# Kernel tuning notes

Measured on AMD Instinct MI355X. Metric: run time of the kernel, lower is better.

## Reference

```python
import jax, jax.numpy as jnp
import numpy as np

B, H, D = 2048, 50, 400          # batch, history_length, news/category embed dim
S, C = 285, 18                   # num_subcategories, num_categories
NC = 50                          # num_clicks_embed_dim (= history_length table size)
FILL = 1e-30                     # masked_fill value used by the original module


def setup_inputs() -> dict:
    key = jax.random.key(0)
    ks = jax.random.split(key, 9)
    vectors = jax.random.normal(ks[0], (B, H, D), dtype=jnp.float32)
    subcategory = jax.random.randint(ks[1], (B, H), 0, S, dtype=jnp.int32)
    category = jax.random.randint(ks[2], (B, H), 0, C, dtype=jnp.int32)
    subcat_embed = jax.random.normal(ks[3], (S, D), dtype=jnp.float32) * 0.02
    cat_embed = jax.random.normal(ks[4], (C, D), dtype=jnp.float32) * 0.02
    clicks_embed = jax.random.normal(ks[5], (H, NC), dtype=jnp.float32) * 0.02
    w_news = jax.random.normal(ks[6], (D,), dtype=jnp.float32) * 0.05
    w_subcat = jax.random.normal(ks[7], (D + NC,), dtype=jnp.float32) * 0.05
    w_cat = jax.random.normal(ks[8], (D + NC,), dtype=jnp.float32) * 0.05
    return {"vectors": vectors, "subcategory": subcategory, "category": category,
            "subcat_embed": subcat_embed, "cat_embed": cat_embed,
            "clicks_embed": clicks_embed, "w_news": w_news,
            "w_subcat": w_subcat, "w_cat": w_cat}


def reference(vectors, subcategory, category, subcat_embed, cat_embed,
              clicks_embed, w_news, w_subcat, w_cat):
    sub_mask = jax.nn.one_hot(subcategory, S, dtype=vectors.dtype)   # [B,H,S]
    cat_mask = jax.nn.one_hot(category, C, dtype=vectors.dtype)      # [B,H,C]
    sub_to_cat = jnp.einsum('bhs,bhc->bsc', sub_mask, cat_mask)      # [B,S,C]

    # --- news -> subcategory attention pooling ---
    news_scores = jnp.einsum('bhd,d->bh', vectors, w_news)           # [B,H]
    scores = jnp.where(sub_mask > 0, news_scores[:, :, None], FILL)  # [B,H,S]
    news_w = jax.nn.softmax(scores, axis=1)
    sub_news_repr = jnp.einsum('bhs,bhd->bsd', news_w, vectors)      # [B,S,D]
    sub_repr = sub_news_repr + subcat_embed[None]                    # [B,S,D]

    sub_clicks = sub_mask.sum(axis=1)                                # [B,S] float counts
    sub_weights = sub_clicks / sub_clicks.sum(axis=1, keepdims=True)
    sub_clicks_emb = clicks_embed[sub_clicks.astype(jnp.int32)]      # [B,S,NC]

    # --- subcategory -> category attention pooling ---
    sc_scores = jnp.einsum('bsk,k->bs',
                           jnp.concatenate([sub_repr, sub_clicks_emb], axis=2),
                           w_subcat)                                 # [B,S]
    scores2 = jnp.where(sub_to_cat > 0, sc_scores[:, :, None], FILL) # [B,S,C]
    sub_w = jax.nn.softmax(scores2, axis=1)
    cat_sub_repr = jnp.einsum('bsc,bsd->bcd', sub_w, sub_repr)       # [B,C,D]
    cat_repr = cat_sub_repr + cat_embed[None]                        # [B,C,D]

    cat_clicks = cat_mask.sum(axis=1)                                # [B,C]
    cat_weights = cat_clicks / cat_clicks.sum(axis=1, keepdims=True)
    cat_clicks_emb = clicks_embed[cat_clicks.astype(jnp.int32)]      # [B,C,NC]

    # --- category -> user attention pooling (unmasked) ---
    c_scores = jnp.einsum('bck,k->bc',
                          jnp.concatenate([cat_repr, cat_clicks_emb], axis=2),
                          w_cat)                                     # [B,C]
    cat_w = jax.nn.softmax(c_scores, axis=1)
    user_repr = jnp.einsum('bc,bcd->bd', cat_w, cat_repr)            # [B,D]

    return (sub_repr, sub_weights, cat_repr, cat_weights, user_repr)
```

## Files before the change

### kernel.cpp

```cpp
#include <hip/hip_runtime.h>

#define BB 2048
#define HH 50
#define DD 400
#define D4 100
#define SS 285
#define CC 18
#define NCC 50
#define FILLV 1e-30f

static constexpr int BLOCK = 256;
static constexpr int TOT4 = SS * D4;

static constexpr size_t OFF1 = (size_t)BB * SS * DD;
static constexpr size_t OFF2 = OFF1 + (size_t)BB * SS;
static constexpr size_t OFF3 = OFF2 + (size_t)BB * CC * DD;
static constexpr size_t OFF4 = OFF3 + (size_t)BB * CC;

#define WS_ETOT 0
#define WS_SCE  400
#define WS_SEW  688
#define WS_CEDS 976
#define WS_CEDC 1026
#define WS_CEW  1076

typedef float f4 __attribute__((ext_vector_type(4)));

__global__ void hierec_pre(const float* __restrict__ subcat_embed,
                           const float* __restrict__ cat_embed,
                           const float* __restrict__ clicks_embed,
                           const float* __restrict__ w_subcat,
                           const float* __restrict__ w_cat,
                           float* __restrict__ ws)
{
    const int tid  = threadIdx.x;
    const int lane = tid & 63;
    const int wave = tid >> 6;
    const int wpb  = blockDim.x >> 6;
    const int gw   = blockIdx.x * wpb + wave;
    const int nw   = gridDim.x * wpb;

    for (int s = gw; s < SS; s += nw) {
        float p1 = 0.f, p2 = 0.f;
        for (int d = lane; d < DD; d += 64) {
            float v = subcat_embed[s * DD + d];
            p1 += v * w_subcat[d];
            p2 += v * w_cat[d];
        }
        for (int off = 32; off; off >>= 1) {
            p1 += __shfl_down(p1, off);
            p2 += __shfl_down(p2, off);
        }
        if (lane == 0) { ws[WS_SCE + s] = p1; ws[WS_SEW + s] = p2; }
    }
    if (blockIdx.x == 0) {
        for (int d = tid; d < DD; d += blockDim.x) {
            float a = 0.f;
            for (int s = 0; s < SS; ++s) a += subcat_embed[s * DD + d];
            ws[WS_ETOT + d] = a;
        }
    }
    if (blockIdx.x == 1) {
        for (int k = wave; k < HH; k += wpb) {
            float p1 = 0.f, p2 = 0.f;
            if (lane < NCC) {
                float v = clicks_embed[k * NCC + lane];
                p1 = v * w_subcat[DD + lane];
                p2 = v * w_cat[DD + lane];
            }
            for (int off = 32; off; off >>= 1) {
                p1 += __shfl_down(p1, off);
                p2 += __shfl_down(p2, off);
            }
            if (lane == 0) { ws[WS_CEDS + k] = p1; ws[WS_CEDC + k] = p2; }
        }
    }
    if (blockIdx.x == 2) {
        for (int c = wave; c < CC; c += wpb) {
            float p = 0.f;
            for (int d = lane; d < DD; d += 64) p += cat_embed[c * DD + d] * w_cat[d];
            for (int off = 32; off; off >>= 1) p += __shfl_down(p, off);
            if (lane == 0) ws[WS_CEW + c] = p;
        }
    }
}

__global__ __launch_bounds__(BLOCK, 8) void hierec_main(
    const float* __restrict__ vectors,
    const int*   __restrict__ subcategory,
    const int*   __restrict__ category,
    const float* __restrict__ subcat_embed,
    const float* __restrict__ cat_embed,
    const float* __restrict__ w_news,
    const float* __restrict__ w_subcat,
    const float* __restrict__ w_cat,
    const float* __restrict__ pre,
    float* __restrict__ out)
{
    const int b    = blockIdx.x;
    const int tid  = threadIdx.x;
    const int lane = tid & 63;
    const int wave = tid >> 6;

    __shared__ f4     vt4L[D4];
    __shared__ f4     et4L[D4];
    __shared__ float  coefS[SS];
    __shared__ unsigned long long maskS[SS];
    __shared__ int    cntS[SS];
    __shared__ float  ns1L[HH], ns2L[HH], ns3L[HH];
    __shared__ float  uzL[HH], wNL[HH], scL[HH];
    __shared__ unsigned long long maskL[HH];
    __shared__ int    hsL[HH], hcL[HH], repL[HH], prepL[HH];
    __shared__ float  GmL[CC][HH];
    __shared__ float  mcL[CC], ucL[CC], rZcL[CC], AL[CC], csL[CC], catwL[CC];
    __shared__ int    cntcL[CC];
    __shared__ int    prepCL[HH], prepSL[HH], prepJL[HH];
    __shared__ float  prepGL[HH], uPL[HH], uGL[HH];
    __shared__ int    npL;
    __shared__ float  PvL, vtwL, etwL, uAL, uEL;

    const float* vb  = vectors + (size_t)b * HH * DD;
    const f4*    vb4 = (const f4*)vb;
    const f4*    se4 = (const f4*)subcat_embed;
    const f4*    ce4 = (const f4*)cat_embed;

    if (tid < HH) {
        hsL[tid] = subcategory[b * HH + tid];
        hcL[tid] = category[b * HH + tid];
    }
    for (int s = tid; s < SS; s += BLOCK) {
        coefS[s] = 1.f / (float)HH;
        maskS[s] = 0ull;
        cntS[s]  = 0;
    }
    __syncthreads();

    for (int h = wave; h < HH; h += 4) {
        float p1 = 0.f, p2 = 0.f, p3 = 0.f;
        for (int d = lane; d < DD; d += 64) {
            float v = vb[h * DD + d];
            p1 += v * w_news[d];
            p2 += v * w_subcat[d];
            p3 += v * w_cat[d];
        }
        for (int off = 32; off; off >>= 1) {
            p1 += __shfl_down(p1, off);
            p2 += __shfl_down(p2, off);
            p3 += __shfl_down(p3, off);
        }
        if (lane == 0) { ns1L[h] = p1; ns2L[h] = p2; ns3L[h] = p3; }
    }
    if (tid < D4) {
        f4 a = {0.f, 0.f, 0.f, 0.f};
        #pragma unroll 5
        for (int h = 0; h < HH; ++h) a += vb4[h * D4 + tid];
        vt4L[tid] = a;
        et4L[tid] = ((const f4*)pre)[tid];
    }
    __syncthreads();

    if (tid < HH) {
        const int h = tid;
        const int s = hsL[h], c = hcL[h];
        unsigned long long mask = 0ull, pmask = 0ull;
        for (int j = 0; j < HH; ++j) {
            bool ms = (hsL[j] == s);
            mask  |= (unsigned long long)(ms ? 1 : 0) << j;
            pmask |= (unsigned long long)((ms && hcL[j] == c) ? 1 : 0) << j;
        }
        int cnt = __popcll(mask);
        bool rep = ((__ffsll((long long)mask) - 1) == h);

        float m = FILLV;
        unsigned long long t = mask;
        while (t) { int j = __ffsll((long long)t) - 1; t &= t - 1; m = fmaxf(m, ns1L[j]); }
        float u = expf(FILLV - m);
        float sumE = 0.f, sum2 = 0.f;
        t = mask;
        while (t) {
            int j = __ffsll((long long)t) - 1; t &= t - 1;
            float e = expf(ns1L[j] - m);
            sumE += e;
            sum2 += (e - u) * ns2L[j];
        }
        float Z = sumE + (float)(HH - cnt) * u;
        float vt2 = 0.f;
        for (int j = 0; j < HH; ++j) vt2 += ns2L[j];
        int ci = cnt < (NCC - 1) ? cnt : (NCC - 1);
        float sc = (sum2 + u * vt2) / Z + pre[WS_SCE + s] + pre[WS_CEDS + ci];

        float e_h = expf(ns1L[h] - m);
        float uz = u / Z;
        wNL[h] = (e_h - u) / Z;
        uzL[h] = uz; maskL[h] = mask; scL[h] = sc;
        repL[h]  = rep ? 1 : 0;
        prepL[h] = ((__ffsll((long long)pmask) - 1) == h) ? 1 : 0;
        if (rep) { coefS[s] = uz; maskS[s] = mask; cntS[s] = cnt; }
    } else if (wave == 1) {
        float p = 0.f;
        const float* et = (const float*)et4L;
        for (int d = lane; d < DD; d += 64) p += et[d] * w_cat[d];
        for (int off = 32; off; off >>= 1) p += __shfl_down(p, off);
        if (lane == 0) etwL = p;
    } else if (wave == 2) {
        float p = (lane < HH) ? ns3L[lane] : 0.f;
        for (int off = 32; off; off >>= 1) p += __shfl_down(p, off);
        if (lane == 0) vtwL = p;
    }
    __syncthreads();

    if (tid < CC) {
        const int c = tid;
        float mc = FILLV; int n = 0, cc2 = 0;
        for (int j = 0; j < HH; ++j) {
            if (hcL[j] == c) ++cc2;
            if (prepL[j] && hcL[j] == c) { ++n; mc = fmaxf(mc, scL[j]); }
        }
        float u = expf(FILLV - mc);
        float sumE = 0.f;
        for (int j = 0; j < HH; ++j)
            if (prepL[j] && hcL[j] == c) sumE += expf(scL[j] - mc);
        float Zc = sumE + (float)(SS - n) * u;
        mcL[c] = mc; ucL[c] = u; rZcL[c] = 1.f / Zc; cntcL[c] = cc2;
        __builtin_nontemporal_store((float)cc2 * (1.f / (float)HH),
                                    &out[OFF3 + (size_t)b * CC + c]);
    }
    if (tid == 64) {
        int nd = 0, np = 0;
        float sumUb = 0.f;
        for (int j = 0; j < HH; ++j) {
            if (repL[j]) { ++nd; sumUb += uzL[j]; }
            if (prepL[j]) { prepCL[np] = hcL[j]; prepSL[np] = hsL[j]; prepJL[np] = j; ++np; }
        }
        npL = np;
        PvL = (float)(SS - nd) * (1.f / (float)HH) + sumUb;
    }
    for (int s = tid; s < SS; s += BLOCK)
        __builtin_nontemporal_store((float)cntS[s] * (1.f / (float)HH),
                                    &out[OFF1 + (size_t)b * SS + s]);
    __syncthreads();

    for (int idx = tid; idx < CC * HH; idx += BLOCK) {
        int c = idx / HH, h = idx - c * HH;
        bool exists = false;
        unsigned long long t = maskL[h];
        while (t) {
            int k = __ffsll((long long)t) - 1; t &= t - 1;
            if (hcL[k] == c) { exists = true; break; }
        }
        float g = exists ? (expf(scL[h] - mcL[c]) - ucL[c]) : 0.f;
        GmL[c][h] = wNL[h] * (ucL[c] + g);
    }
    if (tid < CC) {
        const int c = tid;
        float A = ucL[c] * PvL;
        for (int j = 0; j < HH; ++j)
            if (prepL[j] && hcL[j] == c)
                A += (expf(scL[j] - mcL[c]) - ucL[c]) * uzL[j];
        AL[c] = A;
    }
    __syncthreads();
    if (tid >= 64 && tid < 64 + HH) {
        int jj = tid - 64;
        if (jj < npL) {
            int j = prepJL[jj], c = prepCL[jj];
            prepGL[jj] = expf(scL[j] - mcL[c]) - ucL[c];
        }
    }
    __syncthreads();

    if (tid < CC) {
        const int c = tid;
        float sG = 0.f;
        for (int h = 0; h < HH; ++h) sG += GmL[c][h] * ns3L[h];
        float sP = 0.f;
        const int np = npL;
        for (int jj = 0; jj < np; ++jj)
            if (prepCL[jj] == c) sP += prepGL[jj] * pre[WS_SEW + prepSL[jj]];
        int ci = cntcL[c] < (NCC - 1) ? cntcL[c] : (NCC - 1);
        csL[c] = rZcL[c] * (AL[c] * vtwL + ucL[c] * etwL + sG + sP)
                 + pre[WS_CEW + c] + pre[WS_CEDC + ci];
    }
    __syncthreads();

    if (tid < CC) {
        float m = csL[0];
        for (int j = 1; j < CC; ++j) m = fmaxf(m, csL[j]);
        float Zc = 0.f;
        for (int j = 0; j < CC; ++j) Zc += expf(csL[j] - m);
        catwL[tid] = expf(csL[tid] - m) / Zc;
    }
    __syncthreads();
    if (tid < HH) {
        float g = 0.f;
        for (int c = 0; c < CC; ++c) g += catwL[c] * rZcL[c] * GmL[c][tid];
        uGL[tid] = g;
    }
    if (tid == 64) {
        float uA = 0.f, uE = 0.f;
        for (int c = 0; c < CC; ++c) {
            uA += catwL[c] * rZcL[c] * AL[c];
            uE += catwL[c] * rZcL[c] * ucL[c];
        }
        uAL = uA; uEL = uE;
    }
    if (tid >= 128 && tid < 128 + HH) {
        int jj = tid - 128;
        if (jj < npL) {
            int c = prepCL[jj];
            uPL[jj] = catwL[c] * rZcL[c] * prepGL[jj];
        }
    }
    __syncthreads();


    {
        f4* oc = (f4*)(out + OFF2 + (size_t)b * CC * DD);
        const int np = npL;
        for (int i = tid; i < CC * D4; i += BLOCK) {
            int c = i / D4, q = i - c * D4;
            f4 acc = AL[c] * vt4L[q] + ucL[c] * et4L[q];
            #pragma unroll 5
            for (int h = 0; h < HH; ++h) acc += GmL[c][h] * vb4[h * D4 + q];
            for (int jj = 0; jj < np; ++jj)
                if (prepCL[jj] == c) acc += prepGL[jj] * se4[prepSL[jj] * D4 + q];
            acc = rZcL[c] * acc + ce4[i];
            __builtin_nontemporal_store(acc, &oc[i]);
        }
    }

    {
        f4* ou = (f4*)(out + OFF4 + (size_t)b * DD);
        const int np = npL;
        for (int q = tid; q < D4; q += BLOCK) {
            f4 acc = uAL * vt4L[q] + uEL * et4L[q];
            #pragma unroll 5
            for (int h = 0; h < HH; ++h) acc += uGL[h] * vb4[h * D4 + q];
            for (int jj = 0; jj < np; ++jj) acc += uPL[jj] * se4[prepSL[jj] * D4 + q];
            for (int c = 0; c < CC; ++c) acc += catwL[c] * ce4[c * D4 + q];
            __builtin_nontemporal_store(acc, &ou[q]);
        }
    }

    {
        f4* o4 = (f4*)(out + (size_t)b * SS * DD);
        for (int i = tid; i < TOT4; i += BLOCK) {
            int s = i / D4;
            int q = i - s * D4;
            f4 acc = coefS[s] * vt4L[q] + se4[i];
            unsigned long long t = maskS[s];
            while (t) {
                int j = __ffsll((long long)t) - 1; t &= t - 1;
                acc += wNL[j] * vb4[j * D4 + q];
            }
            __builtin_nontemporal_store(acc, &o4[i]);
        }
    }
}

extern "C" void kernel_launch(void* const* d_in, const int* in_sizes, int n_in,
                              void* d_out, int out_size, void* d_ws, size_t ws_size,
                              hipStream_t stream) {
    const float* vectors      = (const float*)d_in[0];
    const int*   subcategory  = (const int*)d_in[1];
    const int*   category     = (const int*)d_in[2];
    const float* subcat_embed = (const float*)d_in[3];
    const float* cat_embed    = (const float*)d_in[4];
    const float* clicks_embed = (const float*)d_in[5];
    const float* w_news       = (const float*)d_in[6];
    const float* w_subcat     = (const float*)d_in[7];
    const float* w_cat        = (const float*)d_in[8];
    float* out = (float*)d_out;
    float* ws  = (float*)d_ws;

    hipLaunchKernelGGL(hierec_pre, dim3(32), dim3(256), 0, stream,
                       subcat_embed, cat_embed, clicks_embed, w_subcat, w_cat, ws);
    hipLaunchKernelGGL(hierec_main, dim3(BB), dim3(BLOCK), 0, stream,
                       vectors, subcategory, category, subcat_embed, cat_embed,
                       w_news, w_subcat, w_cat, ws, out);
}
```

Baseline: 585.3 us.

## Fuse category and user outputs, vectorize score pass, split clicked/unclicked subcategory writes

The per-history dot products now use float4 loads and also accumulate the column sum of vectors, with the partial sums combined through shared-memory atomics. This removes the separate reduction pass over vectors. The category-representation loop now has threads 0..99 each own one float4 column and process six categories per pass over history, folding the user representation into the same loop so that pass and its extra sync go away. The subcategory output is split into a clicked list, which does masked accumulation, and an unclicked list, which writes a constant-coefficient output, so the mask loop is no longer evaluated for empty subcategories. The trade-offs are that only 100 of 256 threads work in the category phase, the shared-memory float atomics make the summation order nondeterministic, and prepGL is recomputed with an extra search.

```diff
diff --git a/kernel.cpp b/kernel.cpp
--- a/kernel.cpp
+++ b/kernel.cpp
@@ -10,7 +10,6 @@
 #define FILLV 1e-30f
 
 static constexpr int BLOCK = 256;
-static constexpr int TOT4 = SS * D4;
 
 static constexpr size_t OFF1 = (size_t)BB * SS * DD;
 static constexpr size_t OFF2 = OFF1 + (size_t)BB * SS;
@@ -25,6 +24,10 @@
 #define WS_CEW  1076
 
 typedef float f4 __attribute__((ext_vector_type(4)));
+
+__device__ __forceinline__ float dot4(f4 a, f4 b) {
+    return a.x * b.x + a.y * b.y + a.z * b.z + a.w * b.w;
+}
 
 __global__ void hierec_pre(const float* __restrict__ subcat_embed,
                            const float* __restrict__ cat_embed,
@@ -114,10 +117,12 @@
     __shared__ float  GmL[CC][HH];
     __shared__ float  mcL[CC], ucL[CC], rZcL[CC], AL[CC], csL[CC], catwL[CC];
     __shared__ int    cntcL[CC];
-    __shared__ int    prepCL[HH], prepSL[HH], prepJL[HH];
-    __shared__ float  prepGL[HH], uPL[HH], uGL[HH];
-    __shared__ int    npL;
-    __shared__ float  PvL, vtwL, etwL, uAL, uEL;
+    __shared__ int    prepCL[HH], prepSL[HH];
+    __shared__ float  prepGL[HH];
+    __shared__ int    clickedL[HH];
+    __shared__ int    unclkL[SS];
+    __shared__ int    npL, ndL, nUcnt;
+    __shared__ float  PvL, vtwL, etwL;
 
     const float* vb  = vectors + (size_t)b * HH * DD;
     const f4*    vb4 = (const f4*)vb;
@@ -133,29 +138,52 @@
         maskS[s] = 0ull;
         cntS[s]  = 0;
     }
-    __syncthreads();
-
-    for (int h = wave; h < HH; h += 4) {
-        float p1 = 0.f, p2 = 0.f, p3 = 0.f;
-        for (int d = lane; d < DD; d += 64) {
-            float v = vb[h * DD + d];
-            p1 += v * w_news[d];
-            p2 += v * w_subcat[d];
-            p3 += v * w_cat[d];
-        }
-        for (int off = 32; off; off >>= 1) {
-            p1 += __shfl_down(p1, off);
-            p2 += __shfl_down(p2, off);
-            p3 += __shfl_down(p3, off);
-        }
-        if (lane == 0) { ns1L[h] = p1; ns2L[h] = p2; ns3L[h] = p3; }
-    }
     if (tid < D4) {
-        f4 a = {0.f, 0.f, 0.f, 0.f};
-        #pragma unroll 5
-        for (int h = 0; h < HH; ++h) a += vb4[h * D4 + tid];
-        vt4L[tid] = a;
         et4L[tid] = ((const f4*)pre)[tid];
+        f4 z = {0.f, 0.f, 0.f, 0.f};
+        vt4L[tid] = z;
+    }
+    if (tid == 0) nUcnt = 0;
+    __syncthreads();
+
+    {
+        const f4* wn4 = (const f4*)w_news;
+        const f4* ws4 = (const f4*)w_subcat;
+        const f4* wc4 = (const f4*)w_cat;
+        const bool hi = lane < (D4 - 64);
+        f4 vtp0 = {0.f, 0.f, 0.f, 0.f};
+        f4 vtp1 = {0.f, 0.f, 0.f, 0.f};
+        for (int h = wave; h < HH; h += 4) {
+            f4 v0 = __builtin_nontemporal_load(&vb4[h * D4 + lane]);
+            float p1 = dot4(v0, wn4[lane]);
+            float p2 = dot4(v0, ws4[lane]);
+            float p3 = dot4(v0, wc4[lane]);
+            vtp0 += v0;
+            if (hi) {
+                f4 v1 = __builtin_nontemporal_load(&vb4[h * D4 + 64 + lane]);
+                p1 += dot4(v1, wn4[64 + lane]);
+                p2 += dot4(v1, ws4[64 + lane]);
+                p3 += dot4(v1, wc4[64 + lane]);
+                vtp1 += v1;
+            }
+            for (int off = 32; off; off >>= 1) {
+                p1 += __shfl_down(p1, off);
+                p2 += __shfl_down(p2, off);
+                p3 += __shfl_down(p3, off);
+            }
+            if (lane == 0) { ns1L[h] = p1; ns2L[h] = p2; ns3L[h] = p3; }
+        }
+        float* vtf = (float*)vt4L;
+        atomicAdd(&vtf[4 * lane + 0], vtp0.x);
+        atomicAdd(&vtf[4 * lane + 1], vtp0.y);
+        atomicAdd(&vtf[4 * lane + 2], vtp0.z);
+        atomicAdd(&vtf[4 * lane + 3], vtp0.w);
+        if (hi) {
+            atomicAdd(&vtf[4 * (64 + lane) + 0], vtp1.x);
+            atomicAdd(&vtf[4 * (64 + lane) + 1], vtp1.y);
+            atomicAdd(&vtf[4 * (64 + lane) + 2], vtp1.z);
+            atomicAdd(&vtf[4 * (64 + lane) + 3], vtp1.w);
+        }
     }
     __syncthreads();
 
@@ -229,15 +257,20 @@
         int nd = 0, np = 0;
         float sumUb = 0.f;
         for (int j = 0; j < HH; ++j) {
-            if (repL[j]) { ++nd; sumUb += uzL[j]; }
-            if (prepL[j]) { prepCL[np] = hcL[j]; prepSL[np] = hsL[j]; prepJL[np] = j; ++np; }
-        }
-        npL = np;
+            if (repL[j]) { clickedL[nd] = hsL[j]; ++nd; sumUb += uzL[j]; }
+            if (prepL[j]) { prepCL[np] = hcL[j]; prepSL[np] = hsL[j]; ++np; }
+        }
+        npL = np; ndL = nd;
         PvL = (float)(SS - nd) * (1.f / (float)HH) + sumUb;
     }
-    for (int s = tid; s < SS; s += BLOCK)
+    for (int s = tid; s < SS; s += BLOCK) {
         __builtin_nontemporal_store((float)cntS[s] * (1.f / (float)HH),
                                     &out[OFF1 + (size_t)b * SS + s]);
+        if (maskS[s] == 0ull) {
+            int p = atomicAdd(&nUcnt, 1);
+            unclkL[p] = s;
+        }
+    }
     __syncthreads();
 
     for (int idx = tid; idx < CC * HH; idx += BLOCK) {
@@ -259,13 +292,19 @@
                 A += (expf(scL[j] - mcL[c]) - ucL[c]) * uzL[j];
         AL[c] = A;
     }
-    __syncthreads();
     if (tid >= 64 && tid < 64 + HH) {
         int jj = tid - 64;
-        if (jj < npL) {
-            int j = prepJL[jj], c = prepCL[jj];
-            prepGL[jj] = expf(scL[j] - mcL[c]) - ucL[c];
-        }
+        if (jj < HH) {
+        }
+    }
+    __syncthreads();
+    if (tid < HH && tid < npL) {
+        int c = prepCL[tid];
+        int s = prepSL[tid];
+        float g = 0.f;
+        for (int j = 0; j < HH; ++j)
+            if (prepL[j] && hcL[j] == c && hsL[j] == s) { g = expf(scL[j] - mcL[c]) - ucL[c]; break; }
+        prepGL[tid] = g;
     }
     __syncthreads();
 
@@ -291,69 +330,68 @@
         catwL[tid] = expf(csL[tid] - m) / Zc;
     }
     __syncthreads();
-    if (tid < HH) {
-        float g = 0.f;
-        for (int c = 0; c < CC; ++c) g += catwL[c] * rZcL[c] * GmL[c][tid];
-        uGL[tid] = g;
-    }
-    if (tid == 64) {
-        float uA = 0.f, uE = 0.f;
-        for (int c = 0; c < CC; ++c) {
-            uA += catwL[c] * rZcL[c] * AL[c];
-            uE += catwL[c] * rZcL[c] * ucL[c];
-        }
-        uAL = uA; uEL = uE;
-    }
-    if (tid >= 128 && tid < 128 + HH) {
-        int jj = tid - 128;
-        if (jj < npL) {
-            int c = prepCL[jj];
-            uPL[jj] = catwL[c] * rZcL[c] * prepGL[jj];
-        }
-    }
-    __syncthreads();
-
-
+
+
+    if (tid < D4) {
+        const int q = tid;
+        const int np = npL;
+        f4 uacc = {0.f, 0.f, 0.f, 0.f};
+        f4* oc = (f4*)(out + OFF2 + (size_t)b * CC * DD);
+        #pragma unroll 1
+        for (int c0 = 0; c0 < CC; c0 += 6) {
+            f4 vt = vt4L[q], et = et4L[q];
+            f4 a[6];
+            #pragma unroll
+            for (int cc = 0; cc < 6; ++cc) {
+                int c = c0 + cc;
+                a[cc] = AL[c] * vt + ucL[c] * et;
+            }
+            for (int h = 0; h < HH; ++h) {
+                f4 v = __builtin_nontemporal_load(&vb4[h * D4 + q]);
+                #pragma unroll
+                for (int cc = 0; cc < 6; ++cc) a[cc] += GmL[c0 + cc][h] * v;
+            }
+            #pragma unroll
+            for (int cc = 0; cc < 6; ++cc) {
+                int c = c0 + cc;
+                f4 acc = a[cc];
+                for (int jj = 0; jj < np; ++jj)
+                    if (prepCL[jj] == c) acc += prepGL[jj] * se4[prepSL[jj] * D4 + q];
+                acc = rZcL[c] * acc + ce4[c * D4 + q];
+                uacc += catwL[c] * acc;
+                __builtin_nontemporal_store(acc, &oc[c * D4 + q]);
+            }
+        }
+        f4* ou = (f4*)(out + OFF4 + (size_t)b * DD);
+        __builtin_nontemporal_store(uacc, &ou[q]);
+    }
+
+    f4* o4 = (f4*)(out + (size_t)b * SS * DD);
     {
-        f4* oc = (f4*)(out + OFF2 + (size_t)b * CC * DD);
-        const int np = npL;
-        for (int i = tid; i < CC * D4; i += BLOCK) {
-            int c = i / D4, q = i - c * D4;
-            f4 acc = AL[c] * vt4L[q] + ucL[c] * et4L[q];
-            #pragma unroll 5
-            for (int h = 0; h < HH; ++h) acc += GmL[c][h] * vb4[h * D4 + q];
-            for (int jj = 0; jj < np; ++jj)
-                if (prepCL[jj] == c) acc += prepGL[jj] * se4[prepSL[jj] * D4 + q];
-            acc = rZcL[c] * acc + ce4[i];
-            __builtin_nontemporal_store(acc, &oc[i]);
-        }
-    }
-
-    {
-        f4* ou = (f4*)(out + OFF4 + (size_t)b * DD);
-        const int np = npL;
-        for (int q = tid; q < D4; q += BLOCK) {
-            f4 acc = uAL * vt4L[q] + uEL * et4L[q];
-            #pragma unroll 5
-            for (int h = 0; h < HH; ++h) acc += uGL[h] * vb4[h * D4 + q];
-            for (int jj = 0; jj < np; ++jj) acc += uPL[jj] * se4[prepSL[jj] * D4 + q];
-            for (int c = 0; c < CC; ++c) acc += catwL[c] * ce4[c * D4 + q];
-            __builtin_nontemporal_store(acc, &ou[q]);
-        }
-    }
-
-    {
-        f4* o4 = (f4*)(out + (size_t)b * SS * DD);
-        for (int i = tid; i < TOT4; i += BLOCK) {
-            int s = i / D4;
-            int q = i - s * D4;
-            f4 acc = coefS[s] * vt4L[q] + se4[i];
+        const int tot = ndL * D4;
+        for (int i = tid; i < tot; i += BLOCK) {
+            int ii = i / D4;
+            int q  = i - ii * D4;
+            int s  = clickedL[ii];
+            f4 acc = coefS[s] * vt4L[q] + se4[s * D4 + q];
             unsigned long long t = maskS[s];
             while (t) {
                 int j = __ffsll((long long)t) - 1; t &= t - 1;
-                acc += wNL[j] * vb4[j * D4 + q];
-            }
-            __builtin_nontemporal_store(acc, &o4[i]);
+                acc += wNL[j] * __builtin_nontemporal_load(&vb4[j * D4 + q]);
+            }
+            __builtin_nontemporal_store(acc, &o4[s * D4 + q]);
+        }
+    }
+
+    {
+        const int tot = (SS - ndL) * D4;
+        const float cst = 1.f / (float)HH;
+        for (int i = tid; i < tot; i += BLOCK) {
+            int u = i / D4;
+            int q = i - u * D4;
+            int s = unclkL[u];
+            f4 acc = cst * vt4L[q] + se4[s * D4 + q];
+            __builtin_nontemporal_store(acc, &o4[s * D4 + q]);
         }
     }
 }
```

Result: faster. 512.2 us (-12.5%).
